# Performance work log

Measured on AMD Instinct MI355X. Metric: run time of the kernel, lower is better.

## Reference

```python
import jax, jax.numpy as jnp
import numpy as np
from jax import lax


def setup_inputs() -> dict:
    key = jax.random.key(0)
    k1, k2 = jax.random.split(key)
    B, T, C = 8, 4096, 256
    UNITS, WINDOW = 256, 2
    x = jax.random.normal(k1, (B, T, C), dtype=jnp.float32)
    kernel = jax.random.normal(k2, (WINDOW, C, 3 * UNITS), dtype=jnp.float32) * 0.05
    bias = jnp.zeros((3 * UNITS,), dtype=jnp.float32)
    return {"x": x, "kernel": kernel, "bias": bias}


def _qrnn_forward(x, kernel, bias):
    # Causal conv1d: left-pad time axis by (window - 1).
    window = kernel.shape[0]
    xp = jnp.pad(x, ((0, 0), (window - 1, 0), (0, 0)))
    gates = lax.conv_general_dilated(
        xp, kernel, window_strides=(1,), padding='VALID',
        dimension_numbers=('NWC', 'WIO', 'NWC')) + bias
    z, f, o = jnp.split(gates, 3, axis=-1)  # each [B, T, units]
    z = jnp.tanh(z)
    f = jax.nn.sigmoid(f)

    # fo_pool: c_t = f_t * c_{t-1} + (1 - f_t) * z_t, c_0 = 0.
    # Linear recurrence -> associative scan over time with elements (a, b):
    # compose((a1,b1),(a2,b2)) = (a1*a2, a2*b1 + b2).
    def combine(e1, e2):
        a1, b1 = e1
        a2, b2 = e2
        return a1 * a2, a2 * b1 + b2

    _, c = lax.associative_scan(combine, (f, (1.0 - f) * z), axis=1)
    h = jax.nn.sigmoid(o) * c  # output gate
    return h  # return_sequences=True -> [B, T, units]


def reference(x, kernel, bias):
    return _qrnn_forward(x, kernel, bias)
```

## Files before the change

### kernel.cpp

```cpp
#include <hip/hip_runtime.h>
#include <math.h>


#define Bq 8
#define Tq 4096
#define NCq 64
#define Lq 64

typedef __attribute__((ext_vector_type(8))) _Float16 f16x8;
typedef __attribute__((ext_vector_type(4))) float f32x4;

__device__ __forceinline__ float sigmoidf_(float x) {
    return 1.f / (1.f + __expf(-x));
}
__device__ __forceinline__ float tanh_fast(float x) {
    return 1.f - 2.f / (__expf(2.f * x) + 1.f);
}
__device__ __forceinline__ unsigned short f16b(float a) {
    _Float16 h = (_Float16)a;
    return *(unsigned short*)&h;
}
__device__ __forceinline__ unsigned packf(float f) {
    _Float16 h = (_Float16)f;
    _Float16 lo = (_Float16)(f - (float)h);
    return ((unsigned)*(unsigned short*)&h << 16) | *(unsigned short*)&lo;
}
__device__ __forceinline__ float unpackf(unsigned p) {
    unsigned short hu = p >> 16, lu = p & 0xffffu;
    return (float)*(_Float16*)&hu + (float)*(_Float16*)&lu;
}
__device__ __forceinline__ void gload16(const void* g, void* l) {
    __builtin_amdgcn_global_load_lds(
        (const __attribute__((address_space(1))) void*)g,
        (__attribute__((address_space(3))) void*)l, 16, 0, 0);
}

__global__ __launch_bounds__(256) void split_x(
    const float* __restrict__ x, _Float16* __restrict__ xh)
{
    int idx = blockIdx.x * 256 + threadIdx.x;
    if (idx >= Bq * 4097 * 64) return;
    int b  = idx / (4097 * 64);
    int r  = idx % (4097 * 64);
    int tp = r / 64, c4 = (r % 64) << 2;
    size_t o = ((size_t)(b * 4097 + tp) << 8) + c4;
    _Float16 h4[4] = {(_Float16)0.f, (_Float16)0.f, (_Float16)0.f, (_Float16)0.f};
    if (tp > 0) {
        const float4 v = *(const float4*)&x[((size_t)(b * 4096 + tp - 1) << 8) + c4];
        h4[0] = (_Float16)v.x; h4[1] = (_Float16)v.y;
        h4[2] = (_Float16)v.z; h4[3] = (_Float16)v.w;
    }
    *(ushort4*)&xh[o] = *(ushort4*)h4;
}

__global__ __launch_bounds__(256) void split_k(
    const float* __restrict__ kw, _Float16* __restrict__ bh)
{
    int idx = blockIdx.x * 256 + threadIdx.x;
    if (idx >= 768 * 512) return;
    int n = idx >> 9, k = idx & 511;
    bh[((size_t)n << 9) + k] = (_Float16)kw[(size_t)k * 768 + n];
}

__global__ __launch_bounds__(256) void conv_gemm(
    const _Float16* __restrict__ xh, const _Float16* __restrict__ bth,
    const float* __restrict__ bias,
    _Float16* __restrict__ Z, unsigned* __restrict__ Fp, _Float16* __restrict__ SO)
{
    __shared__ _Float16 lds[2][2][4096];
    const int tid = threadIdx.x;
    const int l = tid & 63, w = tid >> 6;
    const int wr = w >> 1, wc = w & 1;
    const int bm = blockIdx.x;
    const int b  = bm >> 5;
    const int t0 = (bm & 31) << 7;
    const int n0 = blockIdx.y << 7;

    f32x4 acc[4][4] = {};

    const int rowT   = tid >> 2;
    const int slotSw = (tid & 3) ^ ((rowT >> 1) & 3);
    size_t gaBase = ((size_t)(b * 4097 + t0 + rowT) << 8) + (slotSw << 3);
    size_t gbBase = ((size_t)(n0 + rowT) << 9) + (slotSw << 3);
    const int ldsW = w << 9;

    int offA[4], offB[4];
    const int colB = (l >> 4) << 4;
    #pragma unroll
    for (int i = 0; i < 4; ++i) {
        int ra = wr * 64 + i * 16 + (l & 15);
        offA[i] = ((ra << 6) + colB) ^ (((ra >> 1) & 3) << 4);
        int rb = wc * 64 + i * 16 + (l & 15);
        offB[i] = ((rb << 6) + colB) ^ (((rb >> 1) & 3) << 4);
    }

    auto stage = [&](int buf, int kk) {
        size_t ga = gaBase + (size_t)kk * 32;
        size_t gb = gbBase + (size_t)kk * 32;
        _Float16* pA = &lds[buf][0][ldsW];
        _Float16* pB = &lds[buf][1][ldsW];
        gload16(xh  + ga,          pA);
        gload16(xh  + ga + 16384,  pA + 2048);
        gload16(bth + gb,          pB);
        gload16(bth + gb + 32768,  pB + 2048);
    };

    auto compute = [&](int buf) {
        const char* bA = (const char*)lds[buf][0];
        const char* bB = (const char*)lds[buf][1];
        f16x8 fa[4], fb[4];
        #pragma unroll
        for (int i = 0; i < 4; ++i) {
            fa[i] = *(const f16x8*)(bA + offA[i]);
            fb[i] = *(const f16x8*)(bB + offB[i]);
        }
        #pragma unroll
        for (int mi = 0; mi < 4; ++mi)
            #pragma unroll
            for (int ni = 0; ni < 4; ++ni)
                acc[mi][ni] = __builtin_amdgcn_mfma_f32_16x16x32_f16(
                    fa[mi], fb[ni], acc[mi][ni], 0, 0, 0);
    };

    stage(0, 0);
    __syncthreads();
    int buf = 0;
    for (int kk = 0; kk < 15; ++kk) {
        stage(buf ^ 1, kk + 1);
        compute(buf);
        __syncthreads();
        buf ^= 1;
    }
    compute(buf);
    __syncthreads();

    const int gsel = (int)(blockIdx.y >> 1);
    float bb[4];
    #pragma unroll
    for (int ni = 0; ni < 4; ++ni)
        bb[ni] = bias[n0 + wc * 64 + ni * 16 + (l & 15)];

    if (gsel == 1) {
        #pragma unroll
        for (int ni = 0; ni < 4; ++ni) {
            const int u = (n0 - 256) + wc * 64 + ni * 16 + (l & 15);
            #pragma unroll
            for (int mi = 0; mi < 4; ++mi)
                #pragma unroll
                for (int r = 0; r < 4; ++r) {
                    const int t = t0 + wr * 64 + mi * 16 + ((l >> 4) << 2) + r;
                    float f = sigmoidf_(acc[mi][ni][r] + bb[ni]);
                    Fp[((size_t)(b * 4096 + t) << 8) + u] = packf(f);
                }
        }
    } else {
        unsigned short* Hd = (unsigned short*)&lds[0][0][0];
        #pragma unroll
        for (int ni = 0; ni < 4; ++ni) {
            const int cl = wc * 64 + ni * 16 + (l & 15);
            #pragma unroll
            for (int mi = 0; mi < 4; ++mi)
                #pragma unroll
                for (int r = 0; r < 4; ++r) {
                    const int trl = wr * 64 + mi * 16 + ((l >> 4) << 2) + r;
                    float g = acc[mi][ni][r] + bb[ni];
                    float a = (gsel == 0) ? tanh_fast(g) : sigmoidf_(g);
                    int byt = (trl << 8) + ((cl << 1) ^ (((trl >> 2) & 3) << 4));
                    *(unsigned short*)((char*)Hd + byt) = f16b(a);
                }
        }
        __syncthreads();
        _Float16* Gg = (gsel == 0) ? Z : SO;
        const int u0 = (gsel == 0) ? n0 : (n0 - 512);
        const size_t gbase = ((size_t)(b * 4096 + t0) << 8) + u0;
        #pragma unroll
        for (int j = 0; j < 8; ++j) {
            int hoff = tid * 8 + j * 2048;
            int row  = hoff >> 7;
            int colB = (hoff & 127) << 1;
            int srcB = (row << 8) + (colB ^ (((row >> 2) & 3) << 4));
            int4 v = *(const int4*)((const char*)Hd + srcB);
            *(int4*)&Gg[gbase + ((size_t)row << 8) + (colB >> 1)] = v;
        }
    }
}

__global__ __launch_bounds__(256) void chunk_reduce(
    const _Float16* __restrict__ Z, const unsigned* __restrict__ Fp,
    float* __restrict__ CA, float* __restrict__ CB)
{
    const int u = threadIdx.x;
    const int blk = blockIdx.x;
    const int b = blk >> 6, ck = blk & 63;
    size_t base = (((size_t)b << 12) + ck * Lq) * 256 + u;
    float A = 1.f, Bv = 0.f;
    #pragma unroll 8
    for (int s = 0; s < Lq; ++s) {
        float f = unpackf(Fp[base + (size_t)s * 256]);
        float z = (float)Z[base + (size_t)s * 256];
        Bv = fmaf(f, Bv, (1.f - f) * z);
        A *= f;
    }
    size_t cidx = ((size_t)b * NCq + ck) * 256 + u;
    CA[cidx] = A;
    CB[cidx] = Bv;
}

__global__ __launch_bounds__(256) void carry_scan(
    const float* __restrict__ CA, const float* __restrict__ CB,
    float* __restrict__ CIN)
{
    const int u = threadIdx.x;
    const int b = blockIdx.x;
    float c = 0.f;
    #pragma unroll 8
    for (int k = 0; k < NCq; ++k) {
        size_t idx = ((size_t)b * NCq + k) * 256 + u;
        CIN[idx] = c;
        c = fmaf(CA[idx], c, CB[idx]);
    }
}

__global__ __launch_bounds__(256) void apply_scan(
    const _Float16* __restrict__ Z, const unsigned* __restrict__ Fp,
    const _Float16* __restrict__ SO, const float* __restrict__ CIN,
    float* __restrict__ out)
{
    const int u = threadIdx.x;
    const int blk = blockIdx.x;
    const int b = blk >> 6, ck = blk & 63;
    float c = CIN[((size_t)b * NCq + ck) * 256 + u];
    size_t base = (((size_t)b << 12) + ck * Lq) * 256 + u;
    #pragma unroll 8
    for (int s = 0; s < Lq; ++s) {
        size_t idx = base + (size_t)s * 256;
        float f = unpackf(Fp[idx]), z = (float)Z[idx];
        c = fmaf(f, c, (1.f - f) * z);
        out[idx] = (float)SO[idx] * c;
    }
}

extern "C" void kernel_launch(void* const* d_in, const int* in_sizes, int n_in,
                              void* d_out, int out_size, void* d_ws, size_t ws_size,
                              hipStream_t stream) {
    const float* x    = (const float*)d_in[0];
    const float* kw   = (const float*)d_in[1];
    const float* bias = (const float*)d_in[2];
    float* out = (float*)d_out;

    char* p = (char*)d_ws;
    _Float16* xh  = (_Float16*)p; p += (size_t)Bq * 4097 * 256 * 2;
    _Float16* bth = (_Float16*)p; p += (size_t)768 * 512 * 2;
    _Float16* Z   = (_Float16*)p; p += (size_t)Bq * Tq * 256 * 2;
    unsigned* Fp  = (unsigned*)p; p += (size_t)Bq * Tq * 256 * 4;
    _Float16* SO  = (_Float16*)p; p += (size_t)Bq * Tq * 256 * 2;
    float* CA  = (float*)p; p += (size_t)Bq * NCq * 256 * 4;
    float* CB  = (float*)p; p += (size_t)Bq * NCq * 256 * 4;
    float* CIN = (float*)p;

    split_x<<<(Bq * 4097 * 64 + 255) / 256, 256, 0, stream>>>(x, xh);
    split_k<<<(768 * 512 + 255) / 256, 256, 0, stream>>>(kw, bth);
    dim3 g1(256, 6);
    conv_gemm<<<g1, 256, 0, stream>>>(xh, bth, bias, Z, Fp, out ? (_Float16*)((char*)d_ws + ((size_t)Bq*4097*256*2 + (size_t)768*512*2 + (size_t)Bq*Tq*256*2 + (size_t)Bq*Tq*256*4)) : nullptr);
    chunk_reduce<<<512, 256, 0, stream>>>(Z, Fp, CA, CB);
    carry_scan<<<Bq, 256, 0, stream>>>(CA, CB, CIN);
    apply_scan<<<512, 256, 0, stream>>>(Z, Fp, SO, CIN, out);
}
```

Before: 93.45 us.

## Store forget gate as fp16 complement and load GEMM weights directly to registers

The forget gate is written as a single fp16 value holding 1-f (computed as sigmoid(-g)) instead of a packed two-half fp32 split. This lets it share the LDS-staged coalesced store path with the other gates and halves its global traffic in the GEMM epilogue and both scan kernels. The GEMM also stops staging the weight operand in LDS, loading it per-lane from global into registers with a fully unrolled double-buffered K loop. Precision of f near zero drops, and direct global B loads may add latency or uncoalesced traffic.

```diff
diff --git a/kernel.cpp b/kernel.cpp
--- a/kernel.cpp
+++ b/kernel.cpp
@@ -19,15 +19,6 @@
 __device__ __forceinline__ unsigned short f16b(float a) {
     _Float16 h = (_Float16)a;
     return *(unsigned short*)&h;
-}
-__device__ __forceinline__ unsigned packf(float f) {
-    _Float16 h = (_Float16)f;
-    _Float16 lo = (_Float16)(f - (float)h);
-    return ((unsigned)*(unsigned short*)&h << 16) | *(unsigned short*)&lo;
-}
-__device__ __forceinline__ float unpackf(unsigned p) {
-    unsigned short hu = p >> 16, lu = p & 0xffffu;
-    return (float)*(_Float16*)&hu + (float)*(_Float16*)&lu;
 }
 __device__ __forceinline__ void gload16(const void* g, void* l) {
     __builtin_amdgcn_global_load_lds(
@@ -65,9 +56,9 @@
 __global__ __launch_bounds__(256) void conv_gemm(
     const _Float16* __restrict__ xh, const _Float16* __restrict__ bth,
     const float* __restrict__ bias,
-    _Float16* __restrict__ Z, unsigned* __restrict__ Fp, _Float16* __restrict__ SO)
-{
-    __shared__ _Float16 lds[2][2][4096];
+    _Float16* __restrict__ Z, _Float16* __restrict__ G, _Float16* __restrict__ SO)
+{
+    __shared__ __align__(16) char smem[32768];
     const int tid = threadIdx.x;
     const int l = tid & 63, w = tid >> 6;
     const int wr = w >> 1, wc = w & 1;
@@ -81,39 +72,37 @@
     const int rowT   = tid >> 2;
     const int slotSw = (tid & 3) ^ ((rowT >> 1) & 3);
     size_t gaBase = ((size_t)(b * 4097 + t0 + rowT) << 8) + (slotSw << 3);
-    size_t gbBase = ((size_t)(n0 + rowT) << 9) + (slotSw << 3);
     const int ldsW = w << 9;
 
-    int offA[4], offB[4];
+    int offA[4];
     const int colB = (l >> 4) << 4;
     #pragma unroll
     for (int i = 0; i < 4; ++i) {
         int ra = wr * 64 + i * 16 + (l & 15);
         offA[i] = ((ra << 6) + colB) ^ (((ra >> 1) & 3) << 4);
-        int rb = wc * 64 + i * 16 + (l & 15);
-        offB[i] = ((rb << 6) + colB) ^ (((rb >> 1) & 3) << 4);
-    }
-
-    auto stage = [&](int buf, int kk) {
+    }
+    size_t bB[4];
+    #pragma unroll
+    for (int ni = 0; ni < 4; ++ni)
+        bB[ni] = ((size_t)(n0 + wc * 64 + ni * 16 + (l & 15)) << 9) + ((l >> 4) << 3);
+
+    auto stageA = [&](int buf, int kk) {
         size_t ga = gaBase + (size_t)kk * 32;
-        size_t gb = gbBase + (size_t)kk * 32;
-        _Float16* pA = &lds[buf][0][ldsW];
-        _Float16* pB = &lds[buf][1][ldsW];
-        gload16(xh  + ga,          pA);
-        gload16(xh  + ga + 16384,  pA + 2048);
-        gload16(bth + gb,          pB);
-        gload16(bth + gb + 32768,  pB + 2048);
+        _Float16* pA = (_Float16*)smem + buf * 4096 + ldsW;
+        gload16(xh + ga,         pA);
+        gload16(xh + ga + 16384, pA + 2048);
     };
-
-    auto compute = [&](int buf) {
-        const char* bA = (const char*)lds[buf][0];
-        const char* bB = (const char*)lds[buf][1];
-        f16x8 fa[4], fb[4];
-        #pragma unroll
-        for (int i = 0; i < 4; ++i) {
+    auto loadB = [&](int kk, f16x8* fb) {
+        #pragma unroll
+        for (int ni = 0; ni < 4; ++ni)
+            fb[ni] = *(const f16x8*)(bth + bB[ni] + (size_t)kk * 32);
+    };
+    auto computeA = [&](int buf, const f16x8* fb) {
+        const char* bA = (const char*)smem + buf * 8192;
+        f16x8 fa[4];
+        #pragma unroll
+        for (int i = 0; i < 4; ++i)
             fa[i] = *(const f16x8*)(bA + offA[i]);
-            fb[i] = *(const f16x8*)(bB + offB[i]);
-        }
         #pragma unroll
         for (int mi = 0; mi < 4; ++mi)
             #pragma unroll
@@ -122,16 +111,22 @@
                     fa[mi], fb[ni], acc[mi][ni], 0, 0, 0);
     };
 
-    stage(0, 0);
+    f16x8 fbA[4], fbB[4];
+    stageA(0, 0);
+    loadB(0, fbA);
     __syncthreads();
-    int buf = 0;
-    for (int kk = 0; kk < 15; ++kk) {
-        stage(buf ^ 1, kk + 1);
-        compute(buf);
-        __syncthreads();
-        buf ^= 1;
-    }
-    compute(buf);
+    #pragma unroll
+    for (int kp = 0; kp < 8; ++kp) {
+        const int k0 = kp * 2;
+        if (k0 + 1 < 16) { stageA(1, k0 + 1); loadB(k0 + 1, fbB); }
+        computeA(0, fbA);
+        if (k0 + 1 < 16) __syncthreads();
+        if (k0 + 1 < 16) {
+            if (k0 + 2 < 16) { stageA(0, k0 + 2); loadB(k0 + 2, fbA); }
+            computeA(1, fbB);
+            if (k0 + 2 < 16) __syncthreads();
+        }
+    }
     __syncthreads();
 
     const int gsel = (int)(blockIdx.y >> 1);
@@ -140,53 +135,40 @@
     for (int ni = 0; ni < 4; ++ni)
         bb[ni] = bias[n0 + wc * 64 + ni * 16 + (l & 15)];
 
-    if (gsel == 1) {
-        #pragma unroll
-        for (int ni = 0; ni < 4; ++ni) {
-            const int u = (n0 - 256) + wc * 64 + ni * 16 + (l & 15);
+    unsigned short* Hd = (unsigned short*)smem;
+    #pragma unroll
+    for (int ni = 0; ni < 4; ++ni) {
+        const int cl = wc * 64 + ni * 16 + (l & 15);
+        #pragma unroll
+        for (int mi = 0; mi < 4; ++mi)
             #pragma unroll
-            for (int mi = 0; mi < 4; ++mi)
-                #pragma unroll
-                for (int r = 0; r < 4; ++r) {
-                    const int t = t0 + wr * 64 + mi * 16 + ((l >> 4) << 2) + r;
-                    float f = sigmoidf_(acc[mi][ni][r] + bb[ni]);
-                    Fp[((size_t)(b * 4096 + t) << 8) + u] = packf(f);
-                }
-        }
-    } else {
-        unsigned short* Hd = (unsigned short*)&lds[0][0][0];
-        #pragma unroll
-        for (int ni = 0; ni < 4; ++ni) {
-            const int cl = wc * 64 + ni * 16 + (l & 15);
-            #pragma unroll
-            for (int mi = 0; mi < 4; ++mi)
-                #pragma unroll
-                for (int r = 0; r < 4; ++r) {
-                    const int trl = wr * 64 + mi * 16 + ((l >> 4) << 2) + r;
-                    float g = acc[mi][ni][r] + bb[ni];
-                    float a = (gsel == 0) ? tanh_fast(g) : sigmoidf_(g);
-                    int byt = (trl << 8) + ((cl << 1) ^ (((trl >> 2) & 3) << 4));
-                    *(unsigned short*)((char*)Hd + byt) = f16b(a);
-                }
-        }
-        __syncthreads();
-        _Float16* Gg = (gsel == 0) ? Z : SO;
-        const int u0 = (gsel == 0) ? n0 : (n0 - 512);
-        const size_t gbase = ((size_t)(b * 4096 + t0) << 8) + u0;
-        #pragma unroll
-        for (int j = 0; j < 8; ++j) {
-            int hoff = tid * 8 + j * 2048;
-            int row  = hoff >> 7;
-            int colB = (hoff & 127) << 1;
-            int srcB = (row << 8) + (colB ^ (((row >> 2) & 3) << 4));
-            int4 v = *(const int4*)((const char*)Hd + srcB);
-            *(int4*)&Gg[gbase + ((size_t)row << 8) + (colB >> 1)] = v;
-        }
+            for (int r = 0; r < 4; ++r) {
+                const int trl = wr * 64 + mi * 16 + ((l >> 4) << 2) + r;
+                float g = acc[mi][ni][r] + bb[ni];
+                float a = (gsel == 0) ? tanh_fast(g)
+                        : (gsel == 1) ? sigmoidf_(-g)
+                                      : sigmoidf_(g);
+                int byt = (trl << 8) + ((cl << 1) ^ (((trl >> 2) & 3) << 4));
+                *(unsigned short*)((char*)Hd + byt) = f16b(a);
+            }
+    }
+    __syncthreads();
+    _Float16* Gg = (gsel == 0) ? Z : (gsel == 1) ? G : SO;
+    const int u0 = n0 & 255;
+    const size_t gbase = ((size_t)(b * 4096 + t0) << 8) + u0;
+    #pragma unroll
+    for (int j = 0; j < 8; ++j) {
+        int hoff = tid * 8 + j * 2048;
+        int row  = hoff >> 7;
+        int cby  = (hoff & 127) << 1;
+        int srcB = (row << 8) + (cby ^ (((row >> 2) & 3) << 4));
+        int4 v = *(const int4*)((const char*)Hd + srcB);
+        *(int4*)&Gg[gbase + ((size_t)row << 8) + (cby >> 1)] = v;
     }
 }
 
 __global__ __launch_bounds__(256) void chunk_reduce(
-    const _Float16* __restrict__ Z, const unsigned* __restrict__ Fp,
+    const _Float16* __restrict__ Z, const _Float16* __restrict__ G,
     float* __restrict__ CA, float* __restrict__ CB)
 {
     const int u = threadIdx.x;
@@ -196,10 +178,11 @@
     float A = 1.f, Bv = 0.f;
     #pragma unroll 8
     for (int s = 0; s < Lq; ++s) {
-        float f = unpackf(Fp[base + (size_t)s * 256]);
-        float z = (float)Z[base + (size_t)s * 256];
-        Bv = fmaf(f, Bv, (1.f - f) * z);
-        A *= f;
+        size_t idx = base + (size_t)s * 256;
+        float g = (float)G[idx];
+        float z = (float)Z[idx];
+        Bv = fmaf(1.f - g, Bv, g * z);
+        A *= (1.f - g);
     }
     size_t cidx = ((size_t)b * NCq + ck) * 256 + u;
     CA[cidx] = A;
@@ -222,7 +205,7 @@
 }
 
 __global__ __launch_bounds__(256) void apply_scan(
-    const _Float16* __restrict__ Z, const unsigned* __restrict__ Fp,
+    const _Float16* __restrict__ Z, const _Float16* __restrict__ G,
     const _Float16* __restrict__ SO, const float* __restrict__ CIN,
     float* __restrict__ out)
 {
@@ -234,8 +217,8 @@
     #pragma unroll 8
     for (int s = 0; s < Lq; ++s) {
         size_t idx = base + (size_t)s * 256;
-        float f = unpackf(Fp[idx]), z = (float)Z[idx];
-        c = fmaf(f, c, (1.f - f) * z);
+        float g = (float)G[idx], z = (float)Z[idx];
+        c = fmaf(1.f - g, c, g * z);
         out[idx] = (float)SO[idx] * c;
     }
 }
@@ -252,7 +235,7 @@
     _Float16* xh  = (_Float16*)p; p += (size_t)Bq * 4097 * 256 * 2;
     _Float16* bth = (_Float16*)p; p += (size_t)768 * 512 * 2;
     _Float16* Z   = (_Float16*)p; p += (size_t)Bq * Tq * 256 * 2;
-    unsigned* Fp  = (unsigned*)p; p += (size_t)Bq * Tq * 256 * 4;
+    _Float16* G   = (_Float16*)p; p += (size_t)Bq * Tq * 256 * 2;
     _Float16* SO  = (_Float16*)p; p += (size_t)Bq * Tq * 256 * 2;
     float* CA  = (float*)p; p += (size_t)Bq * NCq * 256 * 4;
     float* CB  = (float*)p; p += (size_t)Bq * NCq * 256 * 4;
@@ -261,8 +244,8 @@
     split_x<<<(Bq * 4097 * 64 + 255) / 256, 256, 0, stream>>>(x, xh);
     split_k<<<(768 * 512 + 255) / 256, 256, 0, stream>>>(kw, bth);
     dim3 g1(256, 6);
-    conv_gemm<<<g1, 256, 0, stream>>>(xh, bth, bias, Z, Fp, out ? (_Float16*)((char*)d_ws + ((size_t)Bq*4097*256*2 + (size_t)768*512*2 + (size_t)Bq*Tq*256*2 + (size_t)Bq*Tq*256*4)) : nullptr);
-    chunk_reduce<<<512, 256, 0, stream>>>(Z, Fp, CA, CB);
+    conv_gemm<<<g1, 256, 0, stream>>>(xh, bth, bias, Z, G, SO);
+    chunk_reduce<<<512, 256, 0, stream>>>(Z, G, CA, CB);
     carry_scan<<<Bq, 256, 0, stream>>>(CA, CB, CIN);
-    apply_scan<<<512, 256, 0, stream>>>(Z, Fp, SO, CIN, out);
-}
+    apply_scan<<<512, 256, 0, stream>>>(Z, G, SO, CIN, out);
+}
```

Result: slower. 106.2 us (+13.6%).
